# Kernel tuning notes

Hardware: AMD Instinct MI355X
Metric: run time of the kernel (lower is better)

Reference implementation:

```python
import jax, jax.numpy as jnp
import numpy as np

B, C, H, W = 16, 64, 256, 256


def setup_inputs() -> dict:
    key = jax.random.key(0)
    k1, k2 = jax.random.split(key)
    x = jax.random.normal(k1, (B, C, H, W), dtype=jnp.float32)
    # theta near identity so the warp samples mostly in-bounds (realistic STN regime)
    ident = jnp.array([1.0, 0.0, 0.0, 0.0, 1.0, 0.0], dtype=jnp.float32)
    theta = ident[None, :] + 0.1 * jax.random.normal(k2, (B, 6), dtype=jnp.float32)
    return {"x": x, "theta": theta}


def _affine_grid(theta, h, w):
    # F.affine_grid with align_corners=False (torch default):
    # normalized pixel centers in [-1+1/W, 1-1/W]
    xs = (jnp.arange(w, dtype=jnp.float32) + 0.5) * (2.0 / w) - 1.0
    ys = (jnp.arange(h, dtype=jnp.float32) + 0.5) * (2.0 / h) - 1.0
    gx, gy = jnp.meshgrid(xs, ys)  # each [H, W], 'xy' indexing
    base = jnp.stack([gx, gy, jnp.ones_like(gx)], axis=-1)  # [H, W, 3]
    # grid[..., 0] = sampled x coord, grid[..., 1] = sampled y coord
    return jnp.einsum('bij,hwj->bhwi', theta.reshape(-1, 2, 3), base)  # [B, H, W, 2]


def _grid_sample_bilinear_zeros(x, grid):
    # F.grid_sample(mode='bilinear', padding_mode='zeros', align_corners=False)
    b, c, h, w = x.shape
    ix = ((grid[..., 0] + 1.0) * w - 1.0) * 0.5  # [B, H, W] source x (pixel units)
    iy = ((grid[..., 1] + 1.0) * h - 1.0) * 0.5  # [B, H, W] source y
    ix0f = jnp.floor(ix)
    iy0f = jnp.floor(iy)
    tx = ix - ix0f  # fractional offsets (differentiable w.r.t. grid)
    ty = iy - iy0f
    ix0 = ix0f.astype(jnp.int32)
    iy0 = iy0f.astype(jnp.int32)
    ix1 = ix0 + 1
    iy1 = iy0 + 1

    def corner(yi, xi, wgt):
        valid = (xi >= 0) & (xi < w) & (yi >= 0) & (yi < h)
        xc = jnp.clip(xi, 0, w - 1)
        yc = jnp.clip(yi, 0, h - 1)
        # per-batch gather: img[:, yy, xx] -> [C, H, W]
        v = jax.vmap(lambda img, yy, xx: img[:, yy, xx])(x, yc, xc)  # [B, C, H, W]
        return v * (wgt * valid.astype(x.dtype))[:, None, :, :]

    out = (corner(iy0, ix0, (1.0 - tx) * (1.0 - ty))
           + corner(iy0, ix1, tx * (1.0 - ty))
           + corner(iy1, ix0, (1.0 - tx) * ty)
           + corner(iy1, ix1, tx * ty))
    return out


def reference(x, theta):
    grid = _affine_grid(theta, x.shape[2], x.shape[3])
    return _grid_sample_bilinear_zeros(x, grid)
```

## Files before the change

kernel.cpp:

```cpp
#include <hip/hip_runtime.h>


constexpr int B = 16, C = 64, H = 256, W = 256;
constexpr int HW = H * W;
constexpr int CHW = C * HW;

__global__ __launch_bounds__(256) void st_affine_kernel(
    const float* __restrict__ x, const float* __restrict__ theta,
    float* __restrict__ out)
{
    const int tid = blockIdx.x * 256 + threadIdx.x;
    const int b  = tid >> 16;
    const int hw = tid & (HW - 1);
    const int h  = hw >> 8;
    const int w  = hw & (W - 1);

    const float* th = theta + b * 6;
    const float t0 = th[0], t1 = th[1], t2 = th[2];
    const float t3 = th[3], t4 = th[4], t5 = th[5];

    const float gx = (w + 0.5f) * (2.0f / W) - 1.0f;
    const float gy = (h + 0.5f) * (2.0f / H) - 1.0f;

    const float sx = t0 * gx + t1 * gy + t2;
    const float sy = t3 * gx + t4 * gy + t5;

    const float ix = ((sx + 1.0f) * (float)W - 1.0f) * 0.5f;
    const float iy = ((sy + 1.0f) * (float)H - 1.0f) * 0.5f;

    const float ix0f = floorf(ix);
    const float iy0f = floorf(iy);
    const float tx = ix - ix0f;
    const float ty = iy - iy0f;
    const int ix0 = (int)ix0f, iy0 = (int)iy0f;
    const int ix1 = ix0 + 1,   iy1 = iy0 + 1;

    const float vx0 = (ix0 >= 0 && ix0 < W) ? 1.0f : 0.0f;
    const float vx1 = (ix1 >= 0 && ix1 < W) ? 1.0f : 0.0f;
    const float vy0 = (iy0 >= 0 && iy0 < H) ? 1.0f : 0.0f;
    const float vy1 = (iy1 >= 0 && iy1 < H) ? 1.0f : 0.0f;

    const float w00 = (1.0f - tx) * (1.0f - ty) * vx0 * vy0;
    const float w01 = tx          * (1.0f - ty) * vx1 * vy0;
    const float w10 = (1.0f - tx) * ty          * vx0 * vy1;
    const float w11 = tx          * ty          * vx1 * vy1;

    const int cx0 = min(max(ix0, 0), W - 1);
    const int cx1 = min(max(ix1, 0), W - 1);
    const int cy0 = min(max(iy0, 0), H - 1);
    const int cy1 = min(max(iy1, 0), H - 1);

    const int off00 = cy0 * W + cx0;
    const int off01 = cy0 * W + cx1;
    const int off10 = cy1 * W + cx0;
    const int off11 = cy1 * W + cx1;

    const float* __restrict__ xb = x + (size_t)b * CHW;
    float* __restrict__ ob = out + (size_t)b * CHW + hw;

#pragma unroll 4
    for (int c = 0; c < C; ++c) {
        const float* __restrict__ xc = xb + c * HW;
        const float v = xc[off00] * w00 + xc[off01] * w01
                      + xc[off10] * w10 + xc[off11] * w11;
        ob[c * HW] = v;
    }
}

extern "C" void kernel_launch(void* const* d_in, const int* in_sizes, int n_in,
                              void* d_out, int out_size, void* d_ws, size_t ws_size,
                              hipStream_t stream) {
    const float* x     = (const float*)d_in[0];
    const float* theta = (const float*)d_in[1];
    float* out = (float*)d_out;

    const int total = B * HW;
    dim3 grid(total / 256), block(256);
    st_affine_kernel<<<grid, block, 0, stream>>>(x, theta, out);
}
```

Baseline: 543.3 us.

## Process four output rows per thread, swizzle blocks across XCDs, nontemporal stores

Each thread now computes four output rows (HB=4) of one column, holding the precomputed weights and offsets for all four in registers and reusing them across the channel loop. Block IDs are remapped so consecutive row groups land on the same XCD, which should improve L2 locality for neighbouring source rows. Output writes use nontemporal stores so streamed output does not evict input lines from cache. The costs are higher register pressure, fewer blocks in the grid (1024), and more loads in flight per thread.

```diff
diff --git a/kernel.cpp b/kernel.cpp
--- a/kernel.cpp
+++ b/kernel.cpp
@@ -4,66 +4,82 @@
 constexpr int B = 16, C = 64, H = 256, W = 256;
 constexpr int HW = H * W;
 constexpr int CHW = C * HW;
+constexpr int HB = 4;
+constexpr int NBLK = B * (H / HB);
 
 __global__ __launch_bounds__(256) void st_affine_kernel(
     const float* __restrict__ x, const float* __restrict__ theta,
     float* __restrict__ out)
 {
-    const int tid = blockIdx.x * 256 + threadIdx.x;
-    const int b  = tid >> 16;
-    const int hw = tid & (HW - 1);
-    const int h  = hw >> 8;
-    const int w  = hw & (W - 1);
+    const int bid = blockIdx.x;
+    constexpr int CHUNK = NBLK / 8;
+    const int wg = (bid & 7) * CHUNK + (bid >> 3);
+
+    const int b  = wg >> 6;
+    const int h0 = (wg & 63) * HB;
+    const int w  = threadIdx.x;
 
     const float* th = theta + b * 6;
     const float t0 = th[0], t1 = th[1], t2 = th[2];
     const float t3 = th[3], t4 = th[4], t5 = th[5];
 
     const float gx = (w + 0.5f) * (2.0f / W) - 1.0f;
-    const float gy = (h + 0.5f) * (2.0f / H) - 1.0f;
 
-    const float sx = t0 * gx + t1 * gy + t2;
-    const float sy = t3 * gx + t4 * gy + t5;
+    float wt[HB][4];
+    int   off[HB][4];
+#pragma unroll
+    for (int hh = 0; hh < HB; ++hh) {
+        const float gy = (h0 + hh + 0.5f) * (2.0f / H) - 1.0f;
 
-    const float ix = ((sx + 1.0f) * (float)W - 1.0f) * 0.5f;
-    const float iy = ((sy + 1.0f) * (float)H - 1.0f) * 0.5f;
+        const float sx = t0 * gx + t1 * gy + t2;
+        const float sy = t3 * gx + t4 * gy + t5;
 
-    const float ix0f = floorf(ix);
-    const float iy0f = floorf(iy);
-    const float tx = ix - ix0f;
-    const float ty = iy - iy0f;
-    const int ix0 = (int)ix0f, iy0 = (int)iy0f;
-    const int ix1 = ix0 + 1,   iy1 = iy0 + 1;
+        const float ix = ((sx + 1.0f) * (float)W - 1.0f) * 0.5f;
+        const float iy = ((sy + 1.0f) * (float)H - 1.0f) * 0.5f;
 
-    const float vx0 = (ix0 >= 0 && ix0 < W) ? 1.0f : 0.0f;
-    const float vx1 = (ix1 >= 0 && ix1 < W) ? 1.0f : 0.0f;
-    const float vy0 = (iy0 >= 0 && iy0 < H) ? 1.0f : 0.0f;
-    const float vy1 = (iy1 >= 0 && iy1 < H) ? 1.0f : 0.0f;
+        const float ix0f = floorf(ix);
+        const float iy0f = floorf(iy);
+        const float tx = ix - ix0f;
+        const float ty = iy - iy0f;
+        const int ix0 = (int)ix0f, iy0 = (int)iy0f;
+        const int ix1 = ix0 + 1,   iy1 = iy0 + 1;
 
-    const float w00 = (1.0f - tx) * (1.0f - ty) * vx0 * vy0;
-    const float w01 = tx          * (1.0f - ty) * vx1 * vy0;
-    const float w10 = (1.0f - tx) * ty          * vx0 * vy1;
-    const float w11 = tx          * ty          * vx1 * vy1;
+        const float vx0 = (ix0 >= 0 && ix0 < W) ? 1.0f : 0.0f;
+        const float vx1 = (ix1 >= 0 && ix1 < W) ? 1.0f : 0.0f;
+        const float vy0 = (iy0 >= 0 && iy0 < H) ? 1.0f : 0.0f;
+        const float vy1 = (iy1 >= 0 && iy1 < H) ? 1.0f : 0.0f;
 
-    const int cx0 = min(max(ix0, 0), W - 1);
-    const int cx1 = min(max(ix1, 0), W - 1);
-    const int cy0 = min(max(iy0, 0), H - 1);
-    const int cy1 = min(max(iy1, 0), H - 1);
+        wt[hh][0] = (1.0f - tx) * (1.0f - ty) * vx0 * vy0;
+        wt[hh][1] = tx          * (1.0f - ty) * vx1 * vy0;
+        wt[hh][2] = (1.0f - tx) * ty          * vx0 * vy1;
+        wt[hh][3] = tx          * ty          * vx1 * vy1;
 
-    const int off00 = cy0 * W + cx0;
-    const int off01 = cy0 * W + cx1;
-    const int off10 = cy1 * W + cx0;
-    const int off11 = cy1 * W + cx1;
+        const int cx0 = min(max(ix0, 0), W - 1);
+        const int cx1 = min(max(ix1, 0), W - 1);
+        const int cy0 = min(max(iy0, 0), H - 1);
+        const int cy1 = min(max(iy1, 0), H - 1);
+
+        off[hh][0] = cy0 * W + cx0;
+        off[hh][1] = cy0 * W + cx1;
+        off[hh][2] = cy1 * W + cx0;
+        off[hh][3] = cy1 * W + cx1;
+    }
 
     const float* __restrict__ xb = x + (size_t)b * CHW;
-    float* __restrict__ ob = out + (size_t)b * CHW + hw;
+    float* __restrict__ ob = out + (size_t)b * CHW + h0 * W + w;
 
-#pragma unroll 4
+#pragma unroll 2
     for (int c = 0; c < C; ++c) {
         const float* __restrict__ xc = xb + c * HW;
-        const float v = xc[off00] * w00 + xc[off01] * w01
-                      + xc[off10] * w10 + xc[off11] * w11;
-        ob[c * HW] = v;
+        float* __restrict__ oc = ob + (size_t)c * HW;
+#pragma unroll
+        for (int hh = 0; hh < HB; ++hh) {
+            const float v = xc[off[hh][0]] * wt[hh][0]
+                          + xc[off[hh][1]] * wt[hh][1]
+                          + xc[off[hh][2]] * wt[hh][2]
+                          + xc[off[hh][3]] * wt[hh][3];
+            __builtin_nontemporal_store(v, oc + hh * W);
+        }
     }
 }
 
@@ -74,7 +90,6 @@
     const float* theta = (const float*)d_in[1];
     float* out = (float*)d_out;
 
-    const int total = B * HW;
-    dim3 grid(total / 256), block(256);
+    dim3 grid(NBLK), block(256);
     st_affine_kernel<<<grid, block, 0, stream>>>(x, theta, out);
 }
```

New measurement: 558.7 us. 2.8% more time.
